# Kernel tuning notes

Hardware: AMD Instinct MI355X
Metric: run time of the kernel (lower is better)

Reference implementation:

```python
import jax, jax.numpy as jnp
import numpy as np

B, Q, N, D = 16, 64, 16384, 128


def setup_inputs() -> dict:
    key = jax.random.key(0)
    k1, k2, k3 = jax.random.split(key, 3)
    query_vector = jax.random.normal(k1, (B, Q, D), dtype=jnp.float32)
    m_A = jax.random.normal(k2, (B, N, D), dtype=jnp.float32)
    # valid node counts per batch element, in [N//2, N] so masks are non-degenerate
    node_nums = jax.random.randint(k3, (B,), N // 2, N + 1, dtype=jnp.int32)
    return {"query_vector": query_vector, "m_A": m_A, "node_nums": node_nums}


def reference(query_vector, m_A, node_nums):
    # GraphPF.forward with num_supporting_node = -1 (default path).
    # prob_logits: [B, Q, N]
    prob_logits = jnp.einsum("bqd,bnd->bqn", query_vector, m_A)
    neg = jnp.finfo(prob_logits.dtype).min
    # get_attention_mask: additive mask, 0 for valid nodes, finfo.min for padding
    valid = jnp.arange(m_A.shape[1])[None, :] < node_nums[:, None]  # [B, N]
    attention_mask = jnp.where(valid, 0.0, neg).astype(prob_logits.dtype)[:, None, :]
    masked_logits = prob_logits + attention_mask
    prob_soft = jax.nn.softmax(masked_logits, axis=-1)
    res_vector = jnp.einsum("bqn,bnd->bqd", prob_soft, m_A)
    return (res_vector, prob_soft, prob_logits)
```

## Files before the change

kernel.cpp:

```cpp
#include <hip/hip_runtime.h>
#include <math.h>

#define Bn 16
#define Qn 64
#define Nn 16384
#define Dn 128
#define NT 128
#define NTILES (Nn / NT)
#define NCHUNK 256
#define NCHUNKS (Nn / NCHUNK)

#define RES_ELEMS  (Bn * Qn * Dn)
#define SOFT_OFF   (RES_ELEMS)
#define LOG_OFF    (RES_ELEMS + Bn * Qn * Nn)

#define NEGF (-3.4e38f)

typedef __attribute__((ext_vector_type(8))) short short8;
typedef float f32x4 __attribute__((ext_vector_type(4)));

typedef union { unsigned int u[4]; short8 v; } pk8;

__device__ __forceinline__ unsigned int cvt_pk_bf16(float a, float b) {
    unsigned int r;
    asm("v_cvt_pk_bf16_f32 %0, %1, %2" : "=v"(r) : "v"(a), "v"(b));
    return r;
}

__device__ __forceinline__ int swz(int row, int col) {
    return row * 64 + (col ^ ((row & 7) << 3));
}

__global__ __launch_bounds__(256) void k_zero(float* __restrict__ res)
{
    int g = blockIdx.x * 256 + threadIdx.x;
    float4 z; z.x = 0.f; z.y = 0.f; z.z = 0.f; z.w = 0.f;
    ((float4*)res)[g] = z;
}

__global__ __launch_bounds__(256, 3) void k_logits(
    const float* __restrict__ qv, const float* __restrict__ A,
    const int* __restrict__ nodeNum,
    float* __restrict__ logits,
    float* __restrict__ pmax, float* __restrict__ psum)
{
    const int b = blockIdx.y, tile = blockIdx.x;
    const int n0 = tile * NT;
    const int tid = threadIdx.x;
    const int lane = tid & 63, wave = tid >> 6;
    const int qd = lane >> 4, cc = lane & 15;

    __shared__ __align__(16) unsigned char smem[49152];
    unsigned short* QHI = (unsigned short*)smem;
    unsigned short* QLO = QHI + 64 * 64;
    unsigned short* AHI = QLO + 64 * 64;
    unsigned short* ALO = AHI + 128 * 64;
    float* CB   = (float*)smem;
    float* REDM = ((float*)smem) + 64 * 132;
    float* REDS = REDM + 64 * 17;

    f32x4 acc[4][2];
#pragma unroll
    for (int mi = 0; mi < 4; mi++)
#pragma unroll
        for (int ni = 0; ni < 2; ni++) acc[mi][ni] = 0.f;

    const float* qb = qv + (size_t)b * Qn * Dn;
    const float* Ab = A  + (size_t)b * Nn * Dn + (size_t)n0 * Dn;

    const int r16 = tid >> 4, c4 = tid & 15;

    for (int kk = 0; kk < Dn; kk += 64) {
        __syncthreads();
#pragma unroll
        for (int t = 0; t < 4; t++) {
            int row = r16 + 16 * t;
            float4 v = *(const float4*)(qb + (size_t)row * Dn + kk + c4 * 4);
            unsigned int h01 = cvt_pk_bf16(v.x, v.y);
            unsigned int h23 = cvt_pk_bf16(v.z, v.w);
            float rx = v.x - __uint_as_float(h01 << 16);
            float ry = v.y - __uint_as_float(h01 & 0xFFFF0000u);
            float rz = v.z - __uint_as_float(h23 << 16);
            float rw = v.w - __uint_as_float(h23 & 0xFFFF0000u);
            unsigned int l01 = cvt_pk_bf16(rx, ry);
            unsigned int l23 = cvt_pk_bf16(rz, rw);
            int idx = swz(row, c4 * 4);
            uint2 hh; hh.x = h01; hh.y = h23;
            uint2 ll; ll.x = l01; ll.y = l23;
            *(uint2*)(QHI + idx) = hh;
            *(uint2*)(QLO + idx) = ll;
        }
#pragma unroll
        for (int t = 0; t < 8; t++) {
            int row = r16 + 16 * t;
            float4 v = *(const float4*)(Ab + (size_t)row * Dn + kk + c4 * 4);
            unsigned int h01 = cvt_pk_bf16(v.x, v.y);
            unsigned int h23 = cvt_pk_bf16(v.z, v.w);
            float rx = v.x - __uint_as_float(h01 << 16);
            float ry = v.y - __uint_as_float(h01 & 0xFFFF0000u);
            float rz = v.z - __uint_as_float(h23 << 16);
            float rw = v.w - __uint_as_float(h23 & 0xFFFF0000u);
            unsigned int l01 = cvt_pk_bf16(rx, ry);
            unsigned int l23 = cvt_pk_bf16(rz, rw);
            int idx = swz(row, c4 * 4);
            uint2 hh; hh.x = h01; hh.y = h23;
            uint2 ll; ll.x = l01; ll.y = l23;
            *(uint2*)(AHI + idx) = hh;
            *(uint2*)(ALO + idx) = ll;
        }
        __syncthreads();
#pragma unroll
        for (int ks = 0; ks < 64; ks += 32) {
            const int ko = ks + qd * 8;
            short8 qh[4], ql[4], ah[2], al[2];
#pragma unroll
            for (int mi = 0; mi < 4; mi++) {
                int r = mi * 16 + cc;
                int idx = swz(r, ko);
                qh[mi] = *(const short8*)(QHI + idx);
                ql[mi] = *(const short8*)(QLO + idx);
            }
#pragma unroll
            for (int ni = 0; ni < 2; ni++) {
                int r = (wave * 2 + ni) * 16 + cc;
                int idx = swz(r, ko);
                ah[ni] = *(const short8*)(AHI + idx);
                al[ni] = *(const short8*)(ALO + idx);
            }
#pragma unroll
            for (int mi = 0; mi < 4; mi++)
#pragma unroll
                for (int ni = 0; ni < 2; ni++) {
                    acc[mi][ni] = __builtin_amdgcn_mfma_f32_16x16x32_bf16(
                        ql[mi], ah[ni], acc[mi][ni], 0, 0, 0);
                    acc[mi][ni] = __builtin_amdgcn_mfma_f32_16x16x32_bf16(
                        qh[mi], al[ni], acc[mi][ni], 0, 0, 0);
                    acc[mi][ni] = __builtin_amdgcn_mfma_f32_16x16x32_bf16(
                        qh[mi], ah[ni], acc[mi][ni], 0, 0, 0);
                }
        }
    }

    __syncthreads();
#pragma unroll
    for (int mi = 0; mi < 4; mi++)
#pragma unroll
        for (int ni = 0; ni < 2; ni++)
#pragma unroll
            for (int r = 0; r < 4; r++) {
                int q = mi * 16 + qd * 4 + r;
                int n = (wave * 2 + ni) * 16 + cc;
                CB[q * 132 + n] = acc[mi][ni][r];
            }
    __syncthreads();

    const int nv = nodeNum[b];
#pragma unroll
    for (int t = 0; t < 8; t++) {
        int u = tid + t * 256;
        int q = u >> 5, ng = u & 31;
        float4 v = *(const float4*)(CB + q * 132 + ng * 4);
        *(float4*)(logits + ((size_t)(b * Qn + q)) * Nn + n0 + ng * 4) = v;
    }
#pragma unroll
    for (int t = 0; t < 4; t++) {
        int u = tid + t * 256;
        int q = u >> 4, c = u & 15;
        const float* base = CB + q * 132 + c * 8;
        float m = NEGF;
#pragma unroll
        for (int j = 0; j < 8; j++)
            if (n0 + c * 8 + j < nv) m = fmaxf(m, base[j]);
        float s = 0.f;
#pragma unroll
        for (int j = 0; j < 8; j++)
            if (n0 + c * 8 + j < nv) s += __expf(base[j] - m);
        REDM[q * 17 + c] = m;
        REDS[q * 17 + c] = s;
    }
    __syncthreads();
    if (tid < Qn) {
        int q = tid;
        float M = NEGF;
#pragma unroll
        for (int t = 0; t < 16; t++) M = fmaxf(M, REDM[q * 17 + t]);
        float S = 0.f;
#pragma unroll
        for (int t = 0; t < 16; t++)
            S += REDS[q * 17 + t] * __expf(REDM[q * 17 + t] - M);
        pmax[((size_t)(b * Qn + q)) * NTILES + tile] = M;
        psum[((size_t)(b * Qn + q)) * NTILES + tile] = S;
    }
}

__global__ __launch_bounds__(64) void k_rows(
    const float* __restrict__ pmax, const float* __restrict__ psum,
    float* __restrict__ Mrow, float* __restrict__ invL)
{
    const int row = blockIdx.x;
    const int t = threadIdx.x;
    const float* pm = pmax + (size_t)row * NTILES;
    const float* ps = psum + (size_t)row * NTILES;
    float m0 = pm[t], m1 = pm[t + 64];
    float s0 = ps[t], s1 = ps[t + 64];
    float m = fmaxf(m0, m1);
#pragma unroll
    for (int o = 32; o >= 1; o >>= 1) m = fmaxf(m, __shfl_xor(m, o, 64));
    float s = s0 * __expf(m0 - m) + s1 * __expf(m1 - m);
#pragma unroll
    for (int o = 32; o >= 1; o >>= 1) s += __shfl_xor(s, o, 64);
    if (t == 0) { Mrow[row] = m; invL[row] = 1.0f / s; }
}

__global__ __launch_bounds__(256, 4) void k_pv(
    const float* __restrict__ A, const int* __restrict__ nodeNum,
    const float* __restrict__ logits,
    const float* __restrict__ Mrow, const float* __restrict__ invL,
    float* __restrict__ soft, float* __restrict__ res)
{
    const int b = blockIdx.y, chunk = blockIdx.x;
    const int tid = threadIdx.x;
    const int lane = tid & 63, wave = tid >> 6;
    const int qd = lane >> 4, cc = lane & 15;

    __shared__ __align__(16) unsigned short PS[64 * 40];
    __shared__ __align__(16) unsigned int  TMP2[16 * 132];
    __shared__ float MS[64], LS[64];

    if (tid < Qn) {
        MS[tid] = Mrow[b * Qn + tid];
        LS[tid] = invL[b * Qn + tid];
    }

    f32x4 acc[4][2];
#pragma unroll
    for (int mi = 0; mi < 4; mi++)
#pragma unroll
        for (int ni = 0; ni < 2; ni++) acc[mi][ni] = 0.f;

    const int nv = nodeNum[b];
    const float* Abase = A + (size_t)b * Nn * Dn;

    for (int s = 0; s < NCHUNK / 32; s++) {
        const int n0 = chunk * NCHUNK + s * 32;
        __syncthreads();

#pragma unroll
        for (int t = 0; t < 2; t++) {
            int u = tid + t * 256;
            int q = u >> 3, ng = u & 7;
            size_t go = ((size_t)(b * Qn + q)) * Nn + n0 + ng * 4;
            float4 l4 = *(const float4*)(logits + go);
            float mq = MS[q], iq = LS[q];
            int nb = n0 + ng * 4;
            float4 p;
            p.x = (nb + 0 < nv) ? __expf(l4.x - mq) * iq : 0.f;
            p.y = (nb + 1 < nv) ? __expf(l4.y - mq) * iq : 0.f;
            p.z = (nb + 2 < nv) ? __expf(l4.z - mq) * iq : 0.f;
            p.w = (nb + 3 < nv) ? __expf(l4.w - mq) * iq : 0.f;
            *(float4*)(soft + go) = p;
            unsigned int* dst = (unsigned int*)(PS + q * 40 + ng * 4);
            dst[0] = cvt_pk_bf16(p.x, p.y);
            dst[1] = cvt_pk_bf16(p.z, p.w);
        }
#pragma unroll
        for (int t = 0; t < 2; t++) {
            int u = tid + t * 256;
            int n2 = u >> 5, db = u & 31;
            const float* r0 = Abase + (size_t)(n0 + n2 * 2) * Dn + db * 4;
            float4 a0 = *(const float4*)r0;
            float4 a1 = *(const float4*)(r0 + Dn);
            uint4 w;
            w.x = cvt_pk_bf16(a0.x, a1.x);
            w.y = cvt_pk_bf16(a0.y, a1.y);
            w.z = cvt_pk_bf16(a0.z, a1.z);
            w.w = cvt_pk_bf16(a0.w, a1.w);
            *(uint4*)(TMP2 + n2 * 132 + db * 4) = w;
        }
        __syncthreads();

        short8 pf[4];
#pragma unroll
        for (int mi = 0; mi < 4; mi++)
            pf[mi] = *(const short8*)(PS + (mi * 16 + cc) * 40 + qd * 8);
#pragma unroll
        for (int ni = 0; ni < 2; ni++) {
            int d = (wave * 2 + ni) * 16 + cc;
            pk8 bfr;
#pragma unroll
            for (int j = 0; j < 4; j++)
                bfr.u[j] = TMP2[(qd * 4 + j) * 132 + d];
#pragma unroll
            for (int mi = 0; mi < 4; mi++)
                acc[mi][ni] = __builtin_amdgcn_mfma_f32_16x16x32_bf16(
                    pf[mi], bfr.v, acc[mi][ni], 0, 0, 0);
        }
    }

    float* pout = res + (size_t)(b * Qn) * Dn;
#pragma unroll
    for (int mi = 0; mi < 4; mi++)
#pragma unroll
        for (int ni = 0; ni < 2; ni++)
#pragma unroll
            for (int r = 0; r < 4; r++) {
                int q = mi * 16 + qd * 4 + r;
                int d = (wave * 2 + ni) * 16 + cc;
                atomicAdd(&pout[q * Dn + d], acc[mi][ni][r]);
            }
}

extern "C" void kernel_launch(void* const* d_in, const int* in_sizes, int n_in,
                              void* d_out, int out_size, void* d_ws, size_t ws_size,
                              hipStream_t stream) {
    const float* qv = (const float*)d_in[0];
    const float* A  = (const float*)d_in[1];
    const int*   nn = (const int*)d_in[2];

    float* out    = (float*)d_out;
    float* res    = out;
    float* soft   = out + SOFT_OFF;
    float* logits = out + LOG_OFF;

    float* ws      = (float*)d_ws;
    float* pmax    = ws;
    float* psum    = pmax + (size_t)Bn * Qn * NTILES;
    float* Mrow    = psum + (size_t)Bn * Qn * NTILES;
    float* invL    = Mrow + Bn * Qn;

    dim3 blk(256);
    k_zero<<<RES_ELEMS / 1024, blk, 0, stream>>>(res);
    k_logits<<<dim3(NTILES, Bn), blk, 0, stream>>>(qv, A, nn, logits, pmax, psum);
    k_rows<<<Bn * Qn, 64, 0, stream>>>(pmax, psum, Mrow, invL);
    k_pv<<<dim3(NCHUNKS, Bn), blk, 0, stream>>>(A, nn, logits, Mrow, invL, soft, res);
}
```

Before: 290.0 us.

## Replace atomic PV accumulation with per-chunk partials and a reduction kernel

The PV kernel now writes each chunk's partial result to a workspace buffer instead of doing atomicAdd into the output, and a new reduction kernel sums the 64 partials. This also drops the zeroing kernel. The slab per iteration doubles from 32 to 64 nodes so each barrier pair covers more MFMA work, and s_setprio raises wave priority around the MFMA section. The trade-off is extra partial-buffer traffic (about 32 MB written and read back), one extra launch, and larger LDS use per block.

```diff
diff --git a/kernel.cpp b/kernel.cpp
--- a/kernel.cpp
+++ b/kernel.cpp
@@ -9,6 +9,7 @@
 #define NTILES (Nn / NT)
 #define NCHUNK 256
 #define NCHUNKS (Nn / NCHUNK)
+#define SLAB 64
 
 #define RES_ELEMS  (Bn * Qn * Dn)
 #define SOFT_OFF   (RES_ELEMS)
@@ -29,13 +30,6 @@
 
 __device__ __forceinline__ int swz(int row, int col) {
     return row * 64 + (col ^ ((row & 7) << 3));
-}
-
-__global__ __launch_bounds__(256) void k_zero(float* __restrict__ res)
-{
-    int g = blockIdx.x * 256 + threadIdx.x;
-    float4 z; z.x = 0.f; z.y = 0.f; z.z = 0.f; z.w = 0.f;
-    ((float4*)res)[g] = z;
 }
 
 __global__ __launch_bounds__(256, 3) void k_logits(
@@ -216,15 +210,15 @@
     const float* __restrict__ A, const int* __restrict__ nodeNum,
     const float* __restrict__ logits,
     const float* __restrict__ Mrow, const float* __restrict__ invL,
-    float* __restrict__ soft, float* __restrict__ res)
+    float* __restrict__ soft, float* __restrict__ partial)
 {
     const int b = blockIdx.y, chunk = blockIdx.x;
     const int tid = threadIdx.x;
     const int lane = tid & 63, wave = tid >> 6;
     const int qd = lane >> 4, cc = lane & 15;
 
-    __shared__ __align__(16) unsigned short PS[64 * 40];
-    __shared__ __align__(16) unsigned int  TMP2[16 * 132];
+    __shared__ __align__(16) unsigned short PS[64 * 72];
+    __shared__ __align__(16) unsigned int  TMP2[32 * 132];
     __shared__ float MS[64], LS[64];
 
     if (tid < Qn) {
@@ -241,14 +235,14 @@
     const int nv = nodeNum[b];
     const float* Abase = A + (size_t)b * Nn * Dn;
 
-    for (int s = 0; s < NCHUNK / 32; s++) {
-        const int n0 = chunk * NCHUNK + s * 32;
+    for (int s = 0; s < NCHUNK / SLAB; s++) {
+        const int n0 = chunk * NCHUNK + s * SLAB;
         __syncthreads();
 
 #pragma unroll
-        for (int t = 0; t < 2; t++) {
+        for (int t = 0; t < 4; t++) {
             int u = tid + t * 256;
-            int q = u >> 3, ng = u & 7;
+            int q = u >> 4, ng = u & 15;
             size_t go = ((size_t)(b * Qn + q)) * Nn + n0 + ng * 4;
             float4 l4 = *(const float4*)(logits + go);
             float mq = MS[q], iq = LS[q];
@@ -259,12 +253,12 @@
             p.z = (nb + 2 < nv) ? __expf(l4.z - mq) * iq : 0.f;
             p.w = (nb + 3 < nv) ? __expf(l4.w - mq) * iq : 0.f;
             *(float4*)(soft + go) = p;
-            unsigned int* dst = (unsigned int*)(PS + q * 40 + ng * 4);
+            unsigned int* dst = (unsigned int*)(PS + q * 72 + ng * 4);
             dst[0] = cvt_pk_bf16(p.x, p.y);
             dst[1] = cvt_pk_bf16(p.z, p.w);
         }
 #pragma unroll
-        for (int t = 0; t < 2; t++) {
+        for (int t = 0; t < 4; t++) {
             int u = tid + t * 256;
             int n2 = u >> 5, db = u & 31;
             const float* r0 = Abase + (size_t)(n0 + n2 * 2) * Dn + db * 4;
@@ -279,25 +273,30 @@
         }
         __syncthreads();
 
-        short8 pf[4];
-#pragma unroll
-        for (int mi = 0; mi < 4; mi++)
-            pf[mi] = *(const short8*)(PS + (mi * 16 + cc) * 40 + qd * 8);
-#pragma unroll
-        for (int ni = 0; ni < 2; ni++) {
-            int d = (wave * 2 + ni) * 16 + cc;
-            pk8 bfr;
-#pragma unroll
-            for (int j = 0; j < 4; j++)
-                bfr.u[j] = TMP2[(qd * 4 + j) * 132 + d];
+        __builtin_amdgcn_s_setprio(1);
+#pragma unroll
+        for (int ks = 0; ks < 2; ks++) {
+            short8 pf[4];
 #pragma unroll
             for (int mi = 0; mi < 4; mi++)
-                acc[mi][ni] = __builtin_amdgcn_mfma_f32_16x16x32_bf16(
-                    pf[mi], bfr.v, acc[mi][ni], 0, 0, 0);
-        }
-    }
-
-    float* pout = res + (size_t)(b * Qn) * Dn;
+                pf[mi] = *(const short8*)(PS + (mi * 16 + cc) * 72 + ks * 32 + qd * 8);
+#pragma unroll
+            for (int ni = 0; ni < 2; ni++) {
+                int d = (wave * 2 + ni) * 16 + cc;
+                pk8 bfr;
+#pragma unroll
+                for (int j = 0; j < 4; j++)
+                    bfr.u[j] = TMP2[(ks * 16 + qd * 4 + j) * 132 + d];
+#pragma unroll
+                for (int mi = 0; mi < 4; mi++)
+                    acc[mi][ni] = __builtin_amdgcn_mfma_f32_16x16x32_bf16(
+                        pf[mi], bfr.v, acc[mi][ni], 0, 0, 0);
+            }
+        }
+        __builtin_amdgcn_s_setprio(0);
+    }
+
+    float* pout = partial + (size_t)chunk * RES_ELEMS + (size_t)(b * Qn) * Dn;
 #pragma unroll
     for (int mi = 0; mi < 4; mi++)
 #pragma unroll
@@ -306,8 +305,19 @@
             for (int r = 0; r < 4; r++) {
                 int q = mi * 16 + qd * 4 + r;
                 int d = (wave * 2 + ni) * 16 + cc;
-                atomicAdd(&pout[q * Dn + d], acc[mi][ni][r]);
-            }
+                pout[q * Dn + d] = acc[mi][ni][r];
+            }
+}
+
+__global__ __launch_bounds__(256) void k_red(
+    const float* __restrict__ partial, float* __restrict__ res)
+{
+    int g = blockIdx.x * 256 + threadIdx.x;
+    float s = 0.f;
+#pragma unroll
+    for (int t = 0; t < NCHUNKS; t++)
+        s += partial[(size_t)t * RES_ELEMS + g];
+    res[g] = s;
 }
 
 extern "C" void kernel_launch(void* const* d_in, const int* in_sizes, int n_in,
@@ -327,10 +337,11 @@
     float* psum    = pmax + (size_t)Bn * Qn * NTILES;
     float* Mrow    = psum + (size_t)Bn * Qn * NTILES;
     float* invL    = Mrow + Bn * Qn;
+    float* partial = invL + Bn * Qn;
 
     dim3 blk(256);
-    k_zero<<<RES_ELEMS / 1024, blk, 0, stream>>>(res);
     k_logits<<<dim3(NTILES, Bn), blk, 0, stream>>>(qv, A, nn, logits, pmax, psum);
     k_rows<<<Bn * Qn, 64, 0, stream>>>(pmax, psum, Mrow, invL);
-    k_pv<<<dim3(NCHUNKS, Bn), blk, 0, stream>>>(A, nn, logits, Mrow, invL, soft, res);
-}
+    k_pv<<<dim3(NCHUNKS, Bn), blk, 0, stream>>>(A, nn, logits, Mrow, invL, soft, partial);
+    k_red<<<RES_ELEMS / 256, blk, 0, stream>>>(partial, res);
+}
```

After: 305.5 us. 1.05x slower.

## Use single-pass fp16 MFMA for logits and spread PV atomics over 8 copies

Applied to the files above, without the earlier changes.

The logits GEMM moves from a three-pass split-bf16 scheme (hi/lo compensation) to one fp16 MFMA pass. The whole 128-wide K dimension is now staged in LDS at once, which cuts MFMA count and conversion work. Separately, PV atomics are spread across 8 partial result buffers indexed by chunk to reduce atomic contention, and a new reduction kernel sums them. The fp16 path lowers logits precision (round-toward-zero conversion, limited range), which may break tolerance, and it adds extra zeroing, reduction traffic and a launch.

```diff
diff --git a/kernel.cpp b/kernel.cpp
--- a/kernel.cpp
+++ b/kernel.cpp
@@ -9,6 +9,7 @@
 #define NTILES (Nn / NT)
 #define NCHUNK 256
 #define NCHUNKS (Nn / NCHUNK)
+#define NCOPY 8
 
 #define RES_ELEMS  (Bn * Qn * Dn)
 #define SOFT_OFF   (RES_ELEMS)
@@ -17,9 +18,12 @@
 #define NEGF (-3.4e38f)
 
 typedef __attribute__((ext_vector_type(8))) short short8;
+typedef __attribute__((ext_vector_type(8))) _Float16 half8;
+typedef __attribute__((ext_vector_type(2))) __fp16 fp16x2;
 typedef float f32x4 __attribute__((ext_vector_type(4)));
 
 typedef union { unsigned int u[4]; short8 v; } pk8;
+typedef union { fp16x2 h2[2]; ushort4 s; } h4pack;
 
 __device__ __forceinline__ unsigned int cvt_pk_bf16(float a, float b) {
     unsigned int r;
@@ -27,15 +31,15 @@
     return r;
 }
 
-__device__ __forceinline__ int swz(int row, int col) {
-    return row * 64 + (col ^ ((row & 7) << 3));
-}
-
-__global__ __launch_bounds__(256) void k_zero(float* __restrict__ res)
+__device__ __forceinline__ int swz128(int row, int col) {
+    return row * 128 + (col ^ ((row & 7) << 3));
+}
+
+__global__ __launch_bounds__(256) void k_zero(float* __restrict__ partial8)
 {
     int g = blockIdx.x * 256 + threadIdx.x;
     float4 z; z.x = 0.f; z.y = 0.f; z.z = 0.f; z.w = 0.f;
-    ((float4*)res)[g] = z;
+    ((float4*)partial8)[g] = z;
 }
 
 __global__ __launch_bounds__(256, 3) void k_logits(
@@ -51,10 +55,8 @@
     const int qd = lane >> 4, cc = lane & 15;
 
     __shared__ __align__(16) unsigned char smem[49152];
-    unsigned short* QHI = (unsigned short*)smem;
-    unsigned short* QLO = QHI + 64 * 64;
-    unsigned short* AHI = QLO + 64 * 64;
-    unsigned short* ALO = AHI + 128 * 64;
+    unsigned short* QH = (unsigned short*)smem;
+    unsigned short* AH = QH + 64 * 128;
     float* CB   = (float*)smem;
     float* REDM = ((float*)smem) + 64 * 132;
     float* REDS = REDM + 64 * 17;
@@ -68,77 +70,44 @@
     const float* qb = qv + (size_t)b * Qn * Dn;
     const float* Ab = A  + (size_t)b * Nn * Dn + (size_t)n0 * Dn;
 
-    const int r16 = tid >> 4, c4 = tid & 15;
-
-    for (int kk = 0; kk < Dn; kk += 64) {
-        __syncthreads();
-#pragma unroll
-        for (int t = 0; t < 4; t++) {
-            int row = r16 + 16 * t;
-            float4 v = *(const float4*)(qb + (size_t)row * Dn + kk + c4 * 4);
-            unsigned int h01 = cvt_pk_bf16(v.x, v.y);
-            unsigned int h23 = cvt_pk_bf16(v.z, v.w);
-            float rx = v.x - __uint_as_float(h01 << 16);
-            float ry = v.y - __uint_as_float(h01 & 0xFFFF0000u);
-            float rz = v.z - __uint_as_float(h23 << 16);
-            float rw = v.w - __uint_as_float(h23 & 0xFFFF0000u);
-            unsigned int l01 = cvt_pk_bf16(rx, ry);
-            unsigned int l23 = cvt_pk_bf16(rz, rw);
-            int idx = swz(row, c4 * 4);
-            uint2 hh; hh.x = h01; hh.y = h23;
-            uint2 ll; ll.x = l01; ll.y = l23;
-            *(uint2*)(QHI + idx) = hh;
-            *(uint2*)(QLO + idx) = ll;
-        }
-#pragma unroll
-        for (int t = 0; t < 8; t++) {
-            int row = r16 + 16 * t;
-            float4 v = *(const float4*)(Ab + (size_t)row * Dn + kk + c4 * 4);
-            unsigned int h01 = cvt_pk_bf16(v.x, v.y);
-            unsigned int h23 = cvt_pk_bf16(v.z, v.w);
-            float rx = v.x - __uint_as_float(h01 << 16);
-            float ry = v.y - __uint_as_float(h01 & 0xFFFF0000u);
-            float rz = v.z - __uint_as_float(h23 << 16);
-            float rw = v.w - __uint_as_float(h23 & 0xFFFF0000u);
-            unsigned int l01 = cvt_pk_bf16(rx, ry);
-            unsigned int l23 = cvt_pk_bf16(rz, rw);
-            int idx = swz(row, c4 * 4);
-            uint2 hh; hh.x = h01; hh.y = h23;
-            uint2 ll; ll.x = l01; ll.y = l23;
-            *(uint2*)(AHI + idx) = hh;
-            *(uint2*)(ALO + idx) = ll;
-        }
-        __syncthreads();
-#pragma unroll
-        for (int ks = 0; ks < 64; ks += 32) {
-            const int ko = ks + qd * 8;
-            short8 qh[4], ql[4], ah[2], al[2];
-#pragma unroll
-            for (int mi = 0; mi < 4; mi++) {
-                int r = mi * 16 + cc;
-                int idx = swz(r, ko);
-                qh[mi] = *(const short8*)(QHI + idx);
-                ql[mi] = *(const short8*)(QLO + idx);
-            }
-#pragma unroll
-            for (int ni = 0; ni < 2; ni++) {
-                int r = (wave * 2 + ni) * 16 + cc;
-                int idx = swz(r, ko);
-                ah[ni] = *(const short8*)(AHI + idx);
-                al[ni] = *(const short8*)(ALO + idx);
-            }
-#pragma unroll
-            for (int mi = 0; mi < 4; mi++)
-#pragma unroll
-                for (int ni = 0; ni < 2; ni++) {
-                    acc[mi][ni] = __builtin_amdgcn_mfma_f32_16x16x32_bf16(
-                        ql[mi], ah[ni], acc[mi][ni], 0, 0, 0);
-                    acc[mi][ni] = __builtin_amdgcn_mfma_f32_16x16x32_bf16(
-                        qh[mi], al[ni], acc[mi][ni], 0, 0, 0);
-                    acc[mi][ni] = __builtin_amdgcn_mfma_f32_16x16x32_bf16(
-                        qh[mi], ah[ni], acc[mi][ni], 0, 0, 0);
-                }
-        }
+#pragma unroll
+    for (int t = 0; t < 8; t++) {
+        int u = tid + t * 256;
+        int row = u >> 5, c8 = u & 31;
+        float4 v = *(const float4*)(qb + (size_t)row * Dn + c8 * 4);
+        h4pack p;
+        p.h2[0] = __builtin_amdgcn_cvt_pkrtz(v.x, v.y);
+        p.h2[1] = __builtin_amdgcn_cvt_pkrtz(v.z, v.w);
+        *(ushort4*)(QH + swz128(row, c8 * 4)) = p.s;
+    }
+#pragma unroll
+    for (int t = 0; t < 16; t++) {
+        int u = tid + t * 256;
+        int row = u >> 5, c8 = u & 31;
+        float4 v = *(const float4*)(Ab + (size_t)row * Dn + c8 * 4);
+        h4pack p;
+        p.h2[0] = __builtin_amdgcn_cvt_pkrtz(v.x, v.y);
+        p.h2[1] = __builtin_amdgcn_cvt_pkrtz(v.z, v.w);
+        *(ushort4*)(AH + swz128(row, c8 * 4)) = p.s;
+    }
+    __syncthreads();
+
+#pragma unroll
+    for (int ks = 0; ks < 128; ks += 32) {
+        const int ko = ks + qd * 8;
+        half8 qh[4], ah[2];
+#pragma unroll
+        for (int mi = 0; mi < 4; mi++)
+            qh[mi] = *(const half8*)(QH + swz128(mi * 16 + cc, ko));
+#pragma unroll
+        for (int ni = 0; ni < 2; ni++)
+            ah[ni] = *(const half8*)(AH + swz128((wave * 2 + ni) * 16 + cc, ko));
+#pragma unroll
+        for (int mi = 0; mi < 4; mi++)
+#pragma unroll
+            for (int ni = 0; ni < 2; ni++)
+                acc[mi][ni] = __builtin_amdgcn_mfma_f32_16x16x32_f16(
+                    qh[mi], ah[ni], acc[mi][ni], 0, 0, 0);
     }
 
     __syncthreads();
@@ -216,7 +185,7 @@
     const float* __restrict__ A, const int* __restrict__ nodeNum,
     const float* __restrict__ logits,
     const float* __restrict__ Mrow, const float* __restrict__ invL,
-    float* __restrict__ soft, float* __restrict__ res)
+    float* __restrict__ soft, float* __restrict__ partial8)
 {
     const int b = blockIdx.y, chunk = blockIdx.x;
     const int tid = threadIdx.x;
@@ -297,7 +266,8 @@
         }
     }
 
-    float* pout = res + (size_t)(b * Qn) * Dn;
+    float* pout = partial8 + (size_t)(chunk & (NCOPY - 1)) * RES_ELEMS
+                + (size_t)(b * Qn) * Dn;
 #pragma unroll
     for (int mi = 0; mi < 4; mi++)
 #pragma unroll
@@ -308,6 +278,17 @@
                 int d = (wave * 2 + ni) * 16 + cc;
                 atomicAdd(&pout[q * Dn + d], acc[mi][ni][r]);
             }
+}
+
+__global__ __launch_bounds__(256) void k_red8(
+    const float* __restrict__ partial8, float* __restrict__ res)
+{
+    int g = blockIdx.x * 256 + threadIdx.x;
+    float s = 0.f;
+#pragma unroll
+    for (int t = 0; t < NCOPY; t++)
+        s += partial8[(size_t)t * RES_ELEMS + g];
+    res[g] = s;
 }
 
 extern "C" void kernel_launch(void* const* d_in, const int* in_sizes, int n_in,
@@ -327,10 +308,12 @@
     float* psum    = pmax + (size_t)Bn * Qn * NTILES;
     float* Mrow    = psum + (size_t)Bn * Qn * NTILES;
     float* invL    = Mrow + Bn * Qn;
+    float* partial8 = invL + Bn * Qn;
 
     dim3 blk(256);
-    k_zero<<<RES_ELEMS / 1024, blk, 0, stream>>>(res);
+    k_zero<<<(NCOPY * RES_ELEMS) / 1024, blk, 0, stream>>>(partial8);
     k_logits<<<dim3(NTILES, Bn), blk, 0, stream>>>(qv, A, nn, logits, pmax, psum);
     k_rows<<<Bn * Qn, 64, 0, stream>>>(pmax, psum, Mrow, invL);
-    k_pv<<<dim3(NCHUNKS, Bn), blk, 0, stream>>>(A, nn, logits, Mrow, invL, soft, res);
-}
+    k_pv<<<dim3(NCHUNKS, Bn), blk, 0, stream>>>(A, nn, logits, Mrow, invL, soft, partial8);
+    k_red8<<<RES_ELEMS / 256, blk, 0, stream>>>(partial8, res);
+}
```

Result: slower. 296.3 us (+2.2%).
